# Kernel optimization log

Hardware: AMD Instinct MI355X
Metric: run time of the kernel (lower is better)

Reference implementation:

```python
import jax, jax.numpy as jnp
import numpy as np

N, B, FD, D, MSG, SCN, H, FFN = 2048, 16, 128, 32, 32, 16, 4, 64
HD = D // H


def _lin(k, o, i, scale=0.05):
    kw, kb = jax.random.split(k)
    return (jax.random.normal(kw, (o, i), jnp.float32) * scale,
            jax.random.normal(kb, (o,), jnp.float32) * scale)


def setup_inputs() -> dict:
    key = jax.random.key(0)
    ks = jax.random.split(key, 24)
    inp = {}
    inp['src'] = jax.random.randint(ks[0], (B,), 0, N)
    inp['dst'] = jax.random.randint(ks[1], (B,), 0, N)
    inp['edge_feat'] = jax.random.normal(ks[2], (B, 3), jnp.float32)
    inp['timestamps'] = jax.random.uniform(ks[3], (B,), dtype=jnp.float32)
    inp['node_features'] = jax.random.normal(ks[4], (N, FD), jnp.float32)
    inp['adj'] = jnp.zeros((N, N), jnp.float32)  # unused: assume_identity_adj=True
    inp['memory'] = jax.random.normal(ks[5], (N, D), jnp.float32) * 0.1
    inp['W_emb'], inp['b_emb'] = _lin(ks[6], D, FD)
    inp['Wqkv'], inp['bqkv'] = _lin(ks[7], 3 * D, D)
    inp['Wo'], inp['bo'] = _lin(ks[8], D, D)
    inp['g1'] = jnp.ones((D,), jnp.float32); inp['be1'] = jnp.zeros((D,), jnp.float32)
    inp['g2'] = jnp.ones((D,), jnp.float32); inp['be2'] = jnp.zeros((D,), jnp.float32)
    inp['W_f1'], inp['b_f1'] = _lin(ks[9], FFN, D)
    inp['W_f2'], inp['b_f2'] = _lin(ks[10], D, FFN)
    inp['W_scn'], inp['b_scn'] = _lin(ks[11], SCN, D)
    inp['g_scn'] = jnp.ones((SCN,), jnp.float32); inp['be_scn'] = jnp.zeros((SCN,), jnp.float32)
    inp['W_e1'], inp['b_e1'] = _lin(ks[12], 32, 2 * SCN)
    inp['W_e2'], inp['b_e2'] = _lin(ks[13], 16, 32)
    inp['W_e3'], inp['b_e3'] = _lin(ks[14], 1, 16)
    inp['gru_Wih'], inp['gru_bih'] = _lin(ks[15], 3 * D, MSG)
    inp['gru_Whh'], inp['gru_bhh'] = _lin(ks[16], 3 * D, D)
    inp['W_m1'], inp['b_m1'] = _lin(ks[17], MSG, 2 * D + 3)
    inp['W_m2'], inp['b_m2'] = _lin(ks[18], MSG, MSG)
    return inp


def _ln(x, g, b):
    mu = x.mean(-1, keepdims=True)
    var = ((x - mu) ** 2).mean(-1, keepdims=True)
    return (x - mu) * jax.lax.rsqrt(var + 1e-5) * g + b


def _gru(x, h, Wih, Whh, bih, bhh):
    # torch.nn.GRUCell semantics
    gi = x @ Wih.T + bih
    gh = h @ Whh.T + bhh
    ir, iz, i_n = jnp.split(gi, 3, -1)
    hr, hz, h_n = jnp.split(gh, 3, -1)
    r = jax.nn.sigmoid(ir + hr)
    z = jax.nn.sigmoid(iz + hz)
    n = jnp.tanh(i_n + r * h_n)
    return (1.0 - z) * n + z * h


def _update_memory(memory, src, dst, edge_feat,
                   gru_Wih, gru_Whh, gru_bih, gru_bhh, W_m1, b_m1, W_m2, b_m2):
    # messages computed from pre-update memory (as in torch source)
    msg_in = jnp.concatenate([memory[src], memory[dst], edge_feat], axis=1)  # [B, 2D+3]
    messages = jax.nn.relu(msg_in @ W_m1.T + b_m1) @ W_m2.T + b_m2           # [B, MSG]

    def step(mem, inp):
        s, d, m = inp
        hs = _gru(m, mem[s], gru_Wih, gru_Whh, gru_bih, gru_bhh)
        mem = mem.at[s].set(hs)
        hd = _gru(m, mem[d], gru_Wih, gru_Whh, gru_bih, gru_bhh)  # sees updated mem if d==s earlier
        mem = mem.at[d].set(hd)
        return mem, None

    new_mem, _ = jax.lax.scan(step, memory, (src, dst, messages))
    return new_mem


def _edge_logits(node_features, src, dst,
                 W_emb, b_emb, Wqkv, bqkv, Wo, bo, g1, be1, g2, be2,
                 W_f1, b_f1, W_f2, b_f2, W_scn, b_scn, g_scn, be_scn,
                 W_e1, b_e1, W_e2, b_e2, W_e3, b_e3):
    x0 = node_features @ W_emb.T + b_emb                      # [N, D]
    x = jnp.broadcast_to(x0[None], (B, N, D))                 # [B, N, D]
    # --- Graph transformer layer (MHA, eval mode: dropout = identity) ---
    qkv = x @ Wqkv.T + bqkv                                   # [B, N, 3D]
    q, k, v = jnp.split(qkv, 3, -1)
    q = q.reshape(B, N, H, HD)
    k = k.reshape(B, N, H, HD)
    v = v.reshape(B, N, H, HD)
    scores = jnp.einsum('bqhd,bkhd->bhqk', q, k) / np.sqrt(HD)
    attn = jax.nn.softmax(scores, axis=-1)
    ao = jnp.einsum('bhqk,bkhd->bqhd', attn, v).reshape(B, N, D)
    ao = ao @ Wo.T + bo
    x = _ln(x + ao, g1, be1)
    ffn = jax.nn.gelu(x @ W_f1.T + b_f1, approximate=False) @ W_f2.T + b_f2
    x = _ln(x + ffn, g2, be2)
    # --- SCN layer (identity adjacency assumed) ---
    s_out = jax.nn.relu(_ln(x @ W_scn.T + b_scn, g_scn, be_scn))  # [B, N, SCN]
    bi = jnp.arange(B)
    src_emb = s_out[bi, src]
    dst_emb = s_out[bi, dst]
    h = jnp.concatenate([src_emb, dst_emb], axis=-1)
    h = jax.nn.relu(h @ W_e1.T + b_e1)
    h = jax.nn.relu(h @ W_e2.T + b_e2)
    return (h @ W_e3.T + b_e3).squeeze(-1)                    # [B]


def reference(src, dst, edge_feat, timestamps, node_features, adj, memory,
              W_emb, b_emb, Wqkv, bqkv, Wo, bo, g1, be1, g2, be2,
              W_f1, b_f1, W_f2, b_f2, W_scn, b_scn, g_scn, be_scn,
              W_e1, b_e1, W_e2, b_e2, W_e3, b_e3,
              gru_Wih, gru_bih, gru_Whh, gru_bhh, W_m1, b_m1, W_m2, b_m2):
    new_mem = _update_memory(memory, src, dst, edge_feat,
                             gru_Wih, gru_Whh, gru_bih, gru_bhh,
                             W_m1, b_m1, W_m2, b_m2)
    edge_logit = _edge_logits(node_features, src, dst,
                              W_emb, b_emb, Wqkv, bqkv, Wo, bo, g1, be1, g2, be2,
                              W_f1, b_f1, W_f2, b_f2, W_scn, b_scn, g_scn, be_scn,
                              W_e1, b_e1, W_e2, b_e2, W_e3, b_e3)
    return edge_logit, new_mem
```

## Files before the change

### kernel.cpp

```cpp
#include <hip/hip_runtime.h>
#include <math.h>

#define NN   2048
#define BB   16

#define WS_X0   0
#define WS_QT   65536
#define WS_KT   131072
#define WS_VT   196608
#define WS_PART 262144
#define WS_GI   268800
#define WS_FLAG 270336

__device__ __forceinline__ float sigmoidf_(float x) { return 1.0f / (1.0f + __expf(-x)); }
__device__ __forceinline__ float tanhf_(float x) {
    float ex = __expf(2.0f * x);
    return 1.0f - 2.0f / (ex + 1.0f);
}
__device__ __forceinline__ float dot4_(float4 a, float4 b) {
    return a.x*b.x + a.y*b.y + a.z*b.z + a.w*b.w;
}

__global__ __launch_bounds__(256) void kA_embed_qkv_msg(
    const float* __restrict__ nf, const float* __restrict__ Wemb, const float* __restrict__ bemb,
    const float* __restrict__ Wqkv, const float* __restrict__ bqkv,
    const float* __restrict__ mem, const int* __restrict__ src, const int* __restrict__ dst,
    const float* __restrict__ ef,
    const float* __restrict__ Wm1, const float* __restrict__ bm1,
    const float* __restrict__ Wm2, const float* __restrict__ bm2,
    const float* __restrict__ Wih, const float* __restrict__ bih,
    float* __restrict__ ws, float* __restrict__ out)
{
    __shared__ float We_s[32 * 130];
    __shared__ float nf_s[8 * 130];
    __shared__ float x0_s[8 * 33];
    __shared__ float Wq_s[96 * 33];
    __shared__ __align__(16) float Wm1_s[2144];
    __shared__ float Wm2_s[32 * 33];
    __shared__ float Wih_s[96 * 33];
    __shared__ float min_s[67];
    __shared__ float mr_s[32];
    __shared__ float msg_s[32];

    const int t = threadIdx.x, bx = blockIdx.x;
    const bool domsg = (bx < 16);

    float4 rA[4], rB[3], rC;
    #pragma unroll
    for (int k = 0; k < 4; ++k) rA[k] = ((const float4*)Wemb)[t + 256 * k];
    #pragma unroll
    for (int k = 0; k < 3; ++k) rB[k] = ((const float4*)Wqkv)[t + 256 * k];
    rC = ((const float4*)nf)[bx * 256 + t];

    float4 rm1[3], rm2v, rih[3];
    float rminv = 0.f;
    if (domsg) {
        #pragma unroll
        for (int k = 0; k < 3; ++k) {
            int idx = t + 256 * k;
            rm1[k] = (idx < 536) ? ((const float4*)Wm1)[idx] : make_float4(0,0,0,0);
        }
        rm2v = ((const float4*)Wm2)[t];
        #pragma unroll
        for (int k = 0; k < 3; ++k) rih[k] = ((const float4*)Wih)[t + 256 * k];
        if (t < 67) {
            const int e = bx;
            rminv = (t < 32) ? mem[src[e] * 32 + t]
                  : (t < 64) ? mem[dst[e] * 32 + (t - 32)]
                             : ef[e * 3 + (t - 64)];
        }
    }

    if (bx == 255 && t < 128) ((unsigned*)(ws + WS_FLAG))[t] = 0u;
    if (bx >= 16 && bx < 80) {
        int g = (bx - 16) * 256 + t;
        ((float4*)(out + 16))[g] = ((const float4*)mem)[g];
    }

    #pragma unroll
    for (int k = 0; k < 4; ++k) {
        int idx = t + 256 * k;
        int r = idx >> 5, c = (idx & 31) * 4;
        We_s[r * 130 + c] = rA[k].x; We_s[r * 130 + c + 1] = rA[k].y;
        We_s[r * 130 + c + 2] = rA[k].z; We_s[r * 130 + c + 3] = rA[k].w;
    }
    #pragma unroll
    for (int k = 0; k < 3; ++k) {
        int idx = t + 256 * k;
        int r = idx >> 3, c = (idx & 7) * 4;
        Wq_s[r * 33 + c] = rB[k].x; Wq_s[r * 33 + c + 1] = rB[k].y;
        Wq_s[r * 33 + c + 2] = rB[k].z; Wq_s[r * 33 + c + 3] = rB[k].w;
    }
    {
        int r = t >> 5, c = (t & 31) * 4;
        nf_s[r * 130 + c] = rC.x; nf_s[r * 130 + c + 1] = rC.y;
        nf_s[r * 130 + c + 2] = rC.z; nf_s[r * 130 + c + 3] = rC.w;
    }
    if (domsg) {
        #pragma unroll
        for (int k = 0; k < 3; ++k) {
            int idx = t + 256 * k;
            if (idx < 536) ((float4*)Wm1_s)[idx] = rm1[k];
        }
        { int r = t >> 3, c = (t & 7) * 4;
          Wm2_s[r * 33 + c] = rm2v.x; Wm2_s[r * 33 + c + 1] = rm2v.y;
          Wm2_s[r * 33 + c + 2] = rm2v.z; Wm2_s[r * 33 + c + 3] = rm2v.w; }
        #pragma unroll
        for (int k = 0; k < 3; ++k) {
            int idx = t + 256 * k;
            int r = idx >> 3, c = (idx & 7) * 4;
            Wih_s[r * 33 + c] = rih[k].x; Wih_s[r * 33 + c + 1] = rih[k].y;
            Wih_s[r * 33 + c + 2] = rih[k].z; Wih_s[r * 33 + c + 3] = rih[k].w;
        }
        if (t < 67) min_s[t] = rminv;
    }
    __syncthreads();

    const int j = t >> 5, o = t & 31;
    const int n = bx * 8 + j;

    float acc = bemb[o];
    {
        const float2* Wr = (const float2*)&We_s[o * 130];
        const float2* Nr = (const float2*)&nf_s[j * 130];
        float sx = 0.f, sy = 0.f;
        #pragma unroll 16
        for (int i = 0; i < 64; ++i) {
            float2 w = Wr[i], x = Nr[i];
            sx += w.x * x.x; sy += w.y * x.y;
        }
        acc += sx + sy;
    }
    x0_s[j * 33 + o] = acc;
    ws[WS_X0 + n * 32 + o] = acc;
    if (domsg && t < 32) {
        float a1 = bm1[t];
        for (int i = 0; i < 67; ++i) a1 += Wm1_s[t * 67 + i] * min_s[i];
        mr_s[t] = fmaxf(a1, 0.f);
    }
    __syncthreads();

    #pragma unroll
    for (int c = 0; c < 3; ++c) {
        int oo = c * 32 + o;
        float a2 = bqkv[oo];
        #pragma unroll 8
        for (int i = 0; i < 32; ++i) a2 += Wq_s[oo * 33 + i] * x0_s[j * 33 + i];
        int h = o >> 3, d = o & 7;
        float* base = ws + (c == 0 ? WS_QT : (c == 1 ? WS_KT : WS_VT));
        base[h * 16384 + n * 8 + d] = a2;
    }
    if (domsg && t < 32) {
        float a2 = bm2[t];
        #pragma unroll 8
        for (int i = 0; i < 32; ++i) a2 += Wm2_s[t * 33 + i] * mr_s[i];
        msg_s[t] = a2;
    }
    __syncthreads();

    if (domsg && t < 96) {
        float a3 = bih[t];
        #pragma unroll 8
        for (int i = 0; i < 32; ++i) a3 += Wih_s[t * 33 + i] * msg_s[i];
        ws[WS_GI + bx * 96 + t] = a3;
    }
}

__global__ __launch_bounds__(256, 1) void kB_attn_post_scan(
    const int* __restrict__ src, const int* __restrict__ dst,
    const float* __restrict__ mem,
    const float* __restrict__ Wo, const float* __restrict__ bo,
    const float* __restrict__ g1, const float* __restrict__ be1,
    const float* __restrict__ Wf1, const float* __restrict__ bf1,
    const float* __restrict__ Wf2, const float* __restrict__ bf2,
    const float* __restrict__ g2, const float* __restrict__ be2,
    const float* __restrict__ Wscn, const float* __restrict__ bscn,
    const float* __restrict__ gscn, const float* __restrict__ bescn,
    const float* __restrict__ Whh, const float* __restrict__ bhh,
    const float* __restrict__ We1, const float* __restrict__ be1e,
    const float* __restrict__ We2, const float* __restrict__ be2e,
    const float* __restrict__ We3, const float* __restrict__ be3,
    float* __restrict__ ws, float* __restrict__ out)
{
    __shared__ float Wo_s[32 * 33];
    __shared__ float Wf1_s[64 * 33];
    __shared__ float Wf2_s[32 * 65];
    __shared__ float Ws_s[16 * 33];
    __shared__ float arow[32 * 33];
    __shared__ float x1s[32 * 33];
    __shared__ float fs[32 * 65];
    __shared__ float sout_s[32 * 17];
    __shared__ float We1_s[32 * 33];
    __shared__ float We2_s[16 * 33];
    __shared__ float gi_s[16 * 97];
    __shared__ __align__(16) float slots[32 * 36];
    __shared__ int nid_s[32], fid_s[32], last_s[32];

    const int t = threadIdx.x, bx = blockIdx.x;
    unsigned* flags = (unsigned*)(ws + WS_FLAG);

    float4 w1[8], w2[8], w3[8];
    float b1 = 0.f, b2 = 0.f, b3 = 0.f;
    float4 rWo, rF1a, rF1b, rF2a, rF2b, rE1, rWs, rE2, rG0, rG1;
    if (bx == 0) {
        if (t < 64) {
            const int r2 = (t < 32) ? t + 64 : t - 32;
            const int r3 = t + 32;
            #pragma unroll
            for (int c = 0; c < 8; ++c) {
                w1[c] = ((const float4*)Whh)[t * 8 + c];
                w2[c] = ((const float4*)Whh)[r2 * 8 + c];
                w3[c] = ((const float4*)Whh)[r3 * 8 + c];
            }
            b1 = bhh[t]; b2 = bhh[r2]; b3 = bhh[r3];
        }
        rWo  = ((const float4*)Wo)[t];
        rF1a = ((const float4*)Wf1)[t]; rF1b = ((const float4*)Wf1)[t + 256];
        rF2a = ((const float4*)Wf2)[t]; rF2b = ((const float4*)Wf2)[t + 256];
        rE1  = ((const float4*)We1)[t];
        rG0  = ((const float4*)(ws + WS_GI))[t];
        if (t < 128) {
            rWs = ((const float4*)Wscn)[t];
            rE2 = ((const float4*)We2)[t];
            rG1 = ((const float4*)(ws + WS_GI))[t + 256];
        }
        if (t < 32) nid_s[t] = (t & 1) ? dst[t >> 1] : src[t >> 1];
    }

    {
        const int s  = bx >> 2;
        const int ks = bx & 3;
        const int h  = t >> 6;
        const int l  = t & 63;
        const int e = s >> 1;
        const int n = (s & 1) ? dst[e] : src[e];

        const float* qg = ws + WS_QT + h * 16384 + n * 8;
        const float4 qa  = *(const float4*)qg;
        const float4 qb4 = *(const float4*)(qg + 4);
        const float* kbase = ws + WS_KT + h * 16384;
        const float* vbase = ws + WS_VT + h * 16384;

        float4 oa = make_float4(0.f, 0.f, 0.f, 0.f);
        float4 ob = make_float4(0.f, 0.f, 0.f, 0.f);
        float ssum = 0.f;
        const float scale = 0.35355339059327373f;

        #pragma unroll
        for (int i = 0; i < 8; ++i) {
            const int key = ks * 512 + i * 64 + l;
            const float4 ka = *(const float4*)(kbase + key * 8);
            const float4 kb = *(const float4*)(kbase + key * 8 + 4);
            const float sc = (dot4_(qa, ka) + dot4_(qb4, kb)) * scale;
            const float p = __expf(sc);
            ssum += p;
            const float4 va = *(const float4*)(vbase + key * 8);
            const float4 vb = *(const float4*)(vbase + key * 8 + 4);
            oa.x += p * va.x; oa.y += p * va.y; oa.z += p * va.z; oa.w += p * va.w;
            ob.x += p * vb.x; ob.y += p * vb.y; ob.z += p * vb.z; ob.w += p * vb.w;
        }
        #pragma unroll
        for (int m = 1; m <= 32; m <<= 1) {
            ssum += __shfl_xor(ssum, m);
            oa.x += __shfl_xor(oa.x, m); oa.y += __shfl_xor(oa.y, m);
            oa.z += __shfl_xor(oa.z, m); oa.w += __shfl_xor(oa.w, m);
            ob.x += __shfl_xor(ob.x, m); ob.y += __shfl_xor(ob.y, m);
            ob.z += __shfl_xor(ob.z, m); ob.w += __shfl_xor(ob.w, m);
        }
        if (l == 0) {
            float* p = ws + WS_PART + ((s * 4 + h) * 4 + ks) * 12;
            *(float4*)p       = oa;
            *(float4*)(p + 4) = ob;
            p[8] = ssum;
        }
    }
    __threadfence();
    if (t == 0) atomicExch(&flags[bx], 1u);
    if (bx != 0) return;

    if (t < 128) {
        while (atomicAdd(&flags[t], 0u) == 0u) { __builtin_amdgcn_s_sleep(8); }
    }
    __syncthreads();
    __threadfence();

    const int j0 = t >> 5, o = t & 31;

    { int r = t >> 3, c = (t & 7) * 4;
      Wo_s[r * 33 + c] = rWo.x; Wo_s[r * 33 + c + 1] = rWo.y;
      Wo_s[r * 33 + c + 2] = rWo.z; Wo_s[r * 33 + c + 3] = rWo.w;
      We1_s[r * 33 + c] = rE1.x; We1_s[r * 33 + c + 1] = rE1.y;
      We1_s[r * 33 + c + 2] = rE1.z; We1_s[r * 33 + c + 3] = rE1.w;
      Wf1_s[r * 33 + c] = rF1a.x; Wf1_s[r * 33 + c + 1] = rF1a.y;
      Wf1_s[r * 33 + c + 2] = rF1a.z; Wf1_s[r * 33 + c + 3] = rF1a.w;
      int r2 = (t + 256) >> 3, c2 = ((t + 256) & 7) * 4;
      Wf1_s[r2 * 33 + c2] = rF1b.x; Wf1_s[r2 * 33 + c2 + 1] = rF1b.y;
      Wf1_s[r2 * 33 + c2 + 2] = rF1b.z; Wf1_s[r2 * 33 + c2 + 3] = rF1b.w; }
    { int r = t >> 4, c = (t & 15) * 4;
      Wf2_s[r * 65 + c] = rF2a.x; Wf2_s[r * 65 + c + 1] = rF2a.y;
      Wf2_s[r * 65 + c + 2] = rF2a.z; Wf2_s[r * 65 + c + 3] = rF2a.w;
      int r2 = (t + 256) >> 4, c2 = ((t + 256) & 15) * 4;
      Wf2_s[r2 * 65 + c2] = rF2b.x; Wf2_s[r2 * 65 + c2 + 1] = rF2b.y;
      Wf2_s[r2 * 65 + c2 + 2] = rF2b.z; Wf2_s[r2 * 65 + c2 + 3] = rF2b.w; }
    { int f = 4 * t, e = f / 96, off = f - e * 96;
      gi_s[e * 97 + off] = rG0.x; gi_s[e * 97 + off + 1] = rG0.y;
      gi_s[e * 97 + off + 2] = rG0.z; gi_s[e * 97 + off + 3] = rG0.w; }
    if (t < 128) {
        int r = t >> 3, c = (t & 7) * 4;
        Ws_s[r * 33 + c] = rWs.x; Ws_s[r * 33 + c + 1] = rWs.y;
        Ws_s[r * 33 + c + 2] = rWs.z; Ws_s[r * 33 + c + 3] = rWs.w;
        We2_s[r * 33 + c] = rE2.x; We2_s[r * 33 + c + 1] = rE2.y;
        We2_s[r * 33 + c + 2] = rE2.z; We2_s[r * 33 + c + 3] = rE2.w;
        int f = 4 * (t + 256), e2 = f / 96, off = f - e2 * 96;
        gi_s[e2 * 97 + off] = rG1.x; gi_s[e2 * 97 + off + 1] = rG1.y;
        gi_s[e2 * 97 + off + 2] = rG1.z; gi_s[e2 * 97 + off + 3] = rG1.w;
    }

    float x0v[4];
    #pragma unroll
    for (int si = 0; si < 4; ++si) {
        const int jj = si * 8 + j0;
        const int ej = jj >> 1;
        const int n = (jj & 1) ? dst[ej] : src[ej];
        const int h = o >> 3, d = o & 7;
        float num = 0.f, den = 0.f;
        #pragma unroll
        for (int ks = 0; ks < 4; ++ks) {
            const float* p = ws + WS_PART + ((jj * 4 + h) * 4 + ks) * 12;
            num += p[d];
            den += p[8];
        }
        arow[jj * 33 + o] = num / den;
        x0v[si] = ws[WS_X0 + n * 32 + o];
    }
    __syncthreads();

    if (t < 32) {
        int me = nid_s[t], f = t;
        for (int j2 = 0; j2 < t; ++j2) if (nid_s[j2] == me) { f = j2; break; }
        fid_s[t] = f;
        int isl = 1;
        for (int j2 = t + 1; j2 < 32; ++j2) if (nid_s[j2] == me) { isl = 0; break; }
        last_s[t] = isl;
    }
    __syncthreads();

    #pragma unroll
    for (int k = 0; k < 4; ++k) {
        int j2 = j0 + 8 * k;
        if (fid_s[j2] == j2) slots[j2 * 36 + o] = mem[nid_s[j2] * 32 + o];
    }

    #pragma unroll
    for (int si = 0; si < 4; ++si) {
        const int jj = si * 8 + j0;
        float a = bo[o];
        #pragma unroll 8
        for (int i = 0; i < 32; ++i) a += Wo_s[o * 33 + i] * arow[jj * 33 + i];
        float t1 = x0v[si] + a;
        float mu = t1;
        #pragma unroll
        for (int m = 16; m >= 1; m >>= 1) mu += __shfl_xor(mu, m, 32);
        mu *= (1.f / 32.f);
        float dv = t1 - mu;
        float var = dv * dv;
        #pragma unroll
        for (int m = 16; m >= 1; m >>= 1) var += __shfl_xor(var, m, 32);
        var *= (1.f / 32.f);
        x1s[jj * 33 + o] = dv * rsqrtf(var + 1e-5f) * g1[o] + be1[o];
    }
    __syncthreads();

    #pragma unroll
    for (int si = 0; si < 4; ++si) {
        const int jj = si * 8 + j0;
        #pragma unroll
        for (int c = 0; c < 2; ++c) {
            int oo = c * 32 + o;
            float f = bf1[oo];
            #pragma unroll 8
            for (int i = 0; i < 32; ++i) f += Wf1_s[oo * 33 + i] * x1s[jj * 33 + i];
            fs[jj * 65 + oo] = 0.5f * f * (1.f + erff(f * 0.70710678118654752f));
        }
    }
    __syncthreads();

    #pragma unroll
    for (int si = 0; si < 4; ++si) {
        const int jj = si * 8 + j0;
        float f2 = bf2[o];
        #pragma unroll 8
        for (int i = 0; i < 64; ++i) f2 += Wf2_s[o * 65 + i] * fs[jj * 65 + i];
        float t2 = x1s[jj * 33 + o] + f2;
        float mu2 = t2;
        #pragma unroll
        for (int m = 16; m >= 1; m >>= 1) mu2 += __shfl_xor(mu2, m, 32);
        mu2 *= (1.f / 32.f);
        float dv2 = t2 - mu2;
        float var2 = dv2 * dv2;
        #pragma unroll
        for (int m = 16; m >= 1; m >>= 1) var2 += __shfl_xor(var2, m, 32);
        var2 *= (1.f / 32.f);
        x1s[jj * 33 + o] = dv2 * rsqrtf(var2 + 1e-5f) * g2[o] + be2[o];
    }
    __syncthreads();

    if (o < 16) {
        #pragma unroll
        for (int si = 0; si < 4; ++si) {
            const int jj = si * 8 + j0;
            float sc = bscn[o];
            #pragma unroll 8
            for (int i = 0; i < 32; ++i) sc += Ws_s[o * 33 + i] * x1s[jj * 33 + i];
            float m16 = sc;
            #pragma unroll
            for (int m = 8; m >= 1; m >>= 1) m16 += __shfl_xor(m16, m, 16);
            m16 *= (1.f / 16.f);
            float d16 = sc - m16;
            float v16 = d16 * d16;
            #pragma unroll
            for (int m = 8; m >= 1; m >>= 1) v16 += __shfl_xor(v16, m, 16);
            v16 *= (1.f / 16.f);
            float sv = d16 * rsqrtf(v16 + 1e-5f) * gscn[o] + bescn[o];
            sout_s[jj * 17 + o] = fmaxf(sv, 0.f);
        }
    }
    __syncthreads();

    #pragma unroll
    for (int k = 0; k < 2; ++k) {
        int idx = t + 256 * k;
        int e = idx >> 5, i = idx & 31;
        arow[e * 33 + i] = (i < 16) ? sout_s[(2 * e) * 17 + i]
                                    : sout_s[(2 * e + 1) * 17 + (i - 16)];
    }
    __syncthreads();

    #pragma unroll
    for (int k = 0; k < 2; ++k) {
        int e = j0 + 8 * k;
        float acc = be1e[o];
        #pragma unroll 8
        for (int i = 0; i < 32; ++i) acc += We1_s[o * 33 + i] * arow[e * 33 + i];
        fs[e * 33 + o] = fmaxf(acc, 0.f);
    }
    __syncthreads();

    {
        int e = t >> 4, o2 = t & 15;
        float acc = be2e[o2];
        #pragma unroll 8
        for (int i = 0; i < 32; ++i) acc += We2_s[o2 * 33 + i] * fs[e * 33 + i];
        fs[600 + e * 17 + o2] = fmaxf(acc, 0.f);
    }
    __syncthreads();

    if (t < 16) {
        float acc = be3[0];
        #pragma unroll
        for (int i = 0; i < 16; ++i) acc += We3[i] * fs[600 + t * 17 + i];
        out[t] = acc;
    }
    __syncthreads();

    if (t < 64) {
        const bool lowhalf = (t < 32);
        for (int e = 0; e < 16; ++e) {
            const int js = 2 * e, jd = 2 * e + 1;
            const int ss = fid_s[js], sd = fid_s[jd];
            const bool same = (nid_s[js] == nid_s[jd]);
            const int npass = same ? 2 : 1;
            for (int pass = 0; pass < npass; ++pass) {
                const bool do_src = (!same) || (pass == 0);
                const bool do_dst = (!same) || (pass == 1);
                float acc1 = b1, acc2 = b2, acc3 = b3;
                #pragma unroll
                for (int c = 0; c < 8; ++c) {
                    const float4 hs4 = *(const float4*)&slots[ss * 36 + 4 * c];
                    const float4 hd4 = *(const float4*)&slots[sd * 36 + 4 * c];
                    acc1 += dot4_(w1[c], hs4);
                    const float4 hm = lowhalf ? hs4 : hd4;
                    acc2 += dot4_(w2[c], hm);
                    acc3 += dot4_(w3[c], hd4);
                }
                const float shv = __shfl_xor(lowhalf ? acc3 : acc1, 32);
                const float hr = lowhalf ? acc1 : acc2;
                const float hz = shv;
                const float hn = lowhalf ? acc2 : acc3;
                const float ir  = gi_s[e * 97 + o];
                const float iz  = gi_s[e * 97 + 32 + o];
                const float inn = gi_s[e * 97 + 64 + o];
                const float r = sigmoidf_(ir + hr);
                const float z = sigmoidf_(iz + hz);
                const float nn = tanhf_(inn + r * hn);
                const int slot = lowhalf ? ss : sd;
                const float hold = slots[slot * 36 + o];
                const float hnew = (1.f - z) * nn + z * hold;
                const bool wr = lowhalf ? do_src : do_dst;
                if (wr) slots[slot * 36 + o] = hnew;
                __threadfence_block();
            }
        }
    }
    __syncthreads();

    #pragma unroll
    for (int k = 0; k < 4; ++k) {
        int j2 = j0 + 8 * k;
        if (last_s[j2]) out[16 + nid_s[j2] * 32 + o] = slots[fid_s[j2] * 36 + o];
    }
}

extern "C" void kernel_launch(void* const* d_in, const int* in_sizes, int n_in,
                              void* d_out, int out_size, void* d_ws, size_t ws_size,
                              hipStream_t stream)
{
    (void)in_sizes; (void)n_in; (void)out_size; (void)ws_size;
    const int*   src   = (const int*)d_in[0];
    const int*   dst   = (const int*)d_in[1];
    const float* ef    = (const float*)d_in[2];
    const float* nf    = (const float*)d_in[4];
    const float* mem   = (const float*)d_in[6];
    const float* Wemb  = (const float*)d_in[7];
    const float* bemb  = (const float*)d_in[8];
    const float* Wqkv  = (const float*)d_in[9];
    const float* bqkv  = (const float*)d_in[10];
    const float* Wo    = (const float*)d_in[11];
    const float* bo    = (const float*)d_in[12];
    const float* g1    = (const float*)d_in[13];
    const float* be1   = (const float*)d_in[14];
    const float* g2    = (const float*)d_in[15];
    const float* be2   = (const float*)d_in[16];
    const float* Wf1   = (const float*)d_in[17];
    const float* bf1   = (const float*)d_in[18];
    const float* Wf2   = (const float*)d_in[19];
    const float* bf2   = (const float*)d_in[20];
    const float* Wscn  = (const float*)d_in[21];
    const float* bscn  = (const float*)d_in[22];
    const float* gscn  = (const float*)d_in[23];
    const float* bescn = (const float*)d_in[24];
    const float* We1   = (const float*)d_in[25];
    const float* be1e  = (const float*)d_in[26];
    const float* We2   = (const float*)d_in[27];
    const float* be2e  = (const float*)d_in[28];
    const float* We3   = (const float*)d_in[29];
    const float* be3   = (const float*)d_in[30];
    const float* Wih   = (const float*)d_in[31];
    const float* bih   = (const float*)d_in[32];
    const float* Whh   = (const float*)d_in[33];
    const float* bhh   = (const float*)d_in[34];
    const float* Wm1   = (const float*)d_in[35];
    const float* bm1   = (const float*)d_in[36];
    const float* Wm2   = (const float*)d_in[37];
    const float* bm2   = (const float*)d_in[38];
    float* out = (float*)d_out;
    float* ws  = (float*)d_ws;

    hipLaunchKernelGGL(kA_embed_qkv_msg, dim3(256), dim3(256), 0, stream,
        nf, Wemb, bemb, Wqkv, bqkv, mem, src, dst, ef, Wm1, bm1, Wm2, bm2, Wih, bih, ws, out);
    hipLaunchKernelGGL(kB_attn_post_scan, dim3(128), dim3(256), 0, stream,
        src, dst, mem, Wo, bo, g1, be1, Wf1, bf1, Wf2, bf2, g2, be2,
        Wscn, bscn, gscn, bescn, Whh, bhh, We1, be1e, We2, be2e, We3, be3, ws, out);
}
```

Measured before the change: 184.6 us.

## Split attention into its own kernel and parallelize GRU scan by dependency rounds

The fused attention+tail kernel, which used a global flag spin-wait so block 0 could run the serial tail, is split into a separate 128-block attention kernel and a single-block post/scan kernel. This removes the cross-block atomic polling at the cost of an extra launch. The GRU memory update no longer walks 16 edges serially. It now computes dependency rounds per node occurrence and processes all independent slot updates of a round in parallel across the four wavefronts. Small bias vectors are staged in shared memory, and the scan-output shuffle stage is folded into a direct write.

```diff
diff --git a/kernel.cpp b/kernel.cpp
--- a/kernel.cpp
+++ b/kernel.cpp
@@ -10,7 +10,21 @@
 #define WS_VT   196608
 #define WS_PART 262144
 #define WS_GI   268800
-#define WS_FLAG 270336
+
+#define B_BO    0
+#define B_G1    32
+#define B_BE1   64
+#define B_G2    96
+#define B_BE2   128
+#define B_BF1   160
+#define B_BF2   224
+#define B_BSCN  256
+#define B_GSCN  272
+#define B_BESCN 288
+#define B_BE1E  304
+#define B_BE2E  336
+#define B_WE3   352
+#define B_BE3   368
 
 __device__ __forceinline__ float sigmoidf_(float x) { return 1.0f / (1.0f + __expf(-x)); }
 __device__ __forceinline__ float tanhf_(float x) {
@@ -21,7 +35,7 @@
     return a.x*b.x + a.y*b.y + a.z*b.z + a.w*b.w;
 }
 
-__global__ __launch_bounds__(256) void kA_embed_qkv_msg(
+__global__ __launch_bounds__(256) void k1_embed_qkv_msg(
     const float* __restrict__ nf, const float* __restrict__ Wemb, const float* __restrict__ bemb,
     const float* __restrict__ Wqkv, const float* __restrict__ bqkv,
     const float* __restrict__ mem, const int* __restrict__ src, const int* __restrict__ dst,
@@ -71,7 +85,6 @@
         }
     }
 
-    if (bx == 255 && t < 128) ((unsigned*)(ws + WS_FLAG))[t] = 0u;
     if (bx >= 16 && bx < 80) {
         int g = (bx - 16) * 256 + t;
         ((float4*)(out + 16))[g] = ((const float4*)mem)[g];
@@ -166,7 +179,61 @@
     }
 }
 
-__global__ __launch_bounds__(256, 1) void kB_attn_post_scan(
+__global__ __launch_bounds__(256) void k2_attn(
+    const int* __restrict__ src, const int* __restrict__ dst,
+    float* __restrict__ ws)
+{
+    const int t = threadIdx.x, bx = blockIdx.x;
+    const int s  = bx >> 2;
+    const int ks = bx & 3;
+    const int h  = t >> 6;
+    const int l  = t & 63;
+
+    const int e = s >> 1;
+    const int n = (s & 1) ? dst[e] : src[e];
+
+    const float* qg = ws + WS_QT + h * 16384 + n * 8;
+    const float4 qa  = *(const float4*)qg;
+    const float4 qb4 = *(const float4*)(qg + 4);
+    const float* kbase = ws + WS_KT + h * 16384;
+    const float* vbase = ws + WS_VT + h * 16384;
+
+    float4 oa = make_float4(0.f, 0.f, 0.f, 0.f);
+    float4 ob = make_float4(0.f, 0.f, 0.f, 0.f);
+    float ssum = 0.f;
+    const float scale = 0.35355339059327373f;
+
+    #pragma unroll
+    for (int i = 0; i < 8; ++i) {
+        const int key = ks * 512 + i * 64 + l;
+        const float4 ka = *(const float4*)(kbase + key * 8);
+        const float4 kb = *(const float4*)(kbase + key * 8 + 4);
+        const float sc = (dot4_(qa, ka) + dot4_(qb4, kb)) * scale;
+        const float p = __expf(sc);
+        ssum += p;
+        const float4 va = *(const float4*)(vbase + key * 8);
+        const float4 vb = *(const float4*)(vbase + key * 8 + 4);
+        oa.x += p * va.x; oa.y += p * va.y; oa.z += p * va.z; oa.w += p * va.w;
+        ob.x += p * vb.x; ob.y += p * vb.y; ob.z += p * vb.z; ob.w += p * vb.w;
+    }
+
+    #pragma unroll
+    for (int m = 1; m <= 32; m <<= 1) {
+        ssum += __shfl_xor(ssum, m);
+        oa.x += __shfl_xor(oa.x, m); oa.y += __shfl_xor(oa.y, m);
+        oa.z += __shfl_xor(oa.z, m); oa.w += __shfl_xor(oa.w, m);
+        ob.x += __shfl_xor(ob.x, m); ob.y += __shfl_xor(ob.y, m);
+        ob.z += __shfl_xor(ob.z, m); ob.w += __shfl_xor(ob.w, m);
+    }
+    if (l == 0) {
+        float* p = ws + WS_PART + ((s * 4 + h) * 4 + ks) * 12;
+        *(float4*)p       = oa;
+        *(float4*)(p + 4) = ob;
+        p[8] = ssum;
+    }
+}
+
+__global__ __launch_bounds__(256, 1) void k34_post_scan(
     const int* __restrict__ src, const int* __restrict__ dst,
     const float* __restrict__ mem,
     const float* __restrict__ Wo, const float* __restrict__ bo,
@@ -186,105 +253,66 @@
     __shared__ float Wf1_s[64 * 33];
     __shared__ float Wf2_s[32 * 65];
     __shared__ float Ws_s[16 * 33];
+    __shared__ float We1_s[32 * 33];
+    __shared__ float We2_s[16 * 33];
     __shared__ float arow[32 * 33];
     __shared__ float x1s[32 * 33];
     __shared__ float fs[32 * 65];
-    __shared__ float sout_s[32 * 17];
-    __shared__ float We1_s[32 * 33];
-    __shared__ float We2_s[16 * 33];
     __shared__ float gi_s[16 * 97];
     __shared__ __align__(16) float slots[32 * 36];
-    __shared__ int nid_s[32], fid_s[32], last_s[32];
-
-    const int t = threadIdx.x, bx = blockIdx.x;
-    unsigned* flags = (unsigned*)(ws + WS_FLAG);
+    __shared__ float bias_s[384];
+    __shared__ int nid_s[32], prev_s[32], round_s[32], last_s[32];
+    __shared__ int list_s[32], cnt_s, maxr_s;
+
+    const int t = threadIdx.x;
+    const int j0 = t >> 5, o = t & 31;
+    const int l = t & 63, w = t >> 6;
+    const bool lowhalf = (l < 32);
 
     float4 w1[8], w2[8], w3[8];
-    float b1 = 0.f, b2 = 0.f, b3 = 0.f;
+    {
+        const int r2 = lowhalf ? l + 64 : l - 32;
+        const int r3 = l + 32;
+        #pragma unroll
+        for (int c = 0; c < 8; ++c) {
+            w1[c] = ((const float4*)Whh)[l * 8 + c];
+            w2[c] = ((const float4*)Whh)[r2 * 8 + c];
+            w3[c] = ((const float4*)Whh)[r3 * 8 + c];
+        }
+    }
+    const float b1 = bhh[l], b2 = bhh[lowhalf ? l + 64 : l - 32], b3 = bhh[l + 32];
+
     float4 rWo, rF1a, rF1b, rF2a, rF2b, rE1, rWs, rE2, rG0, rG1;
-    if (bx == 0) {
-        if (t < 64) {
-            const int r2 = (t < 32) ? t + 64 : t - 32;
-            const int r3 = t + 32;
-            #pragma unroll
-            for (int c = 0; c < 8; ++c) {
-                w1[c] = ((const float4*)Whh)[t * 8 + c];
-                w2[c] = ((const float4*)Whh)[r2 * 8 + c];
-                w3[c] = ((const float4*)Whh)[r3 * 8 + c];
-            }
-            b1 = bhh[t]; b2 = bhh[r2]; b3 = bhh[r3];
-        }
-        rWo  = ((const float4*)Wo)[t];
-        rF1a = ((const float4*)Wf1)[t]; rF1b = ((const float4*)Wf1)[t + 256];
-        rF2a = ((const float4*)Wf2)[t]; rF2b = ((const float4*)Wf2)[t + 256];
-        rE1  = ((const float4*)We1)[t];
-        rG0  = ((const float4*)(ws + WS_GI))[t];
-        if (t < 128) {
-            rWs = ((const float4*)Wscn)[t];
-            rE2 = ((const float4*)We2)[t];
-            rG1 = ((const float4*)(ws + WS_GI))[t + 256];
-        }
-        if (t < 32) nid_s[t] = (t & 1) ? dst[t >> 1] : src[t >> 1];
-    }
-
-    {
-        const int s  = bx >> 2;
-        const int ks = bx & 3;
-        const int h  = t >> 6;
-        const int l  = t & 63;
-        const int e = s >> 1;
-        const int n = (s & 1) ? dst[e] : src[e];
-
-        const float* qg = ws + WS_QT + h * 16384 + n * 8;
-        const float4 qa  = *(const float4*)qg;
-        const float4 qb4 = *(const float4*)(qg + 4);
-        const float* kbase = ws + WS_KT + h * 16384;
-        const float* vbase = ws + WS_VT + h * 16384;
-
-        float4 oa = make_float4(0.f, 0.f, 0.f, 0.f);
-        float4 ob = make_float4(0.f, 0.f, 0.f, 0.f);
-        float ssum = 0.f;
-        const float scale = 0.35355339059327373f;
-
-        #pragma unroll
-        for (int i = 0; i < 8; ++i) {
-            const int key = ks * 512 + i * 64 + l;
-            const float4 ka = *(const float4*)(kbase + key * 8);
-            const float4 kb = *(const float4*)(kbase + key * 8 + 4);
-            const float sc = (dot4_(qa, ka) + dot4_(qb4, kb)) * scale;
-            const float p = __expf(sc);
-            ssum += p;
-            const float4 va = *(const float4*)(vbase + key * 8);
-            const float4 vb = *(const float4*)(vbase + key * 8 + 4);
-            oa.x += p * va.x; oa.y += p * va.y; oa.z += p * va.z; oa.w += p * va.w;
-            ob.x += p * vb.x; ob.y += p * vb.y; ob.z += p * vb.z; ob.w += p * vb.w;
-        }
-        #pragma unroll
-        for (int m = 1; m <= 32; m <<= 1) {
-            ssum += __shfl_xor(ssum, m);
-            oa.x += __shfl_xor(oa.x, m); oa.y += __shfl_xor(oa.y, m);
-            oa.z += __shfl_xor(oa.z, m); oa.w += __shfl_xor(oa.w, m);
-            ob.x += __shfl_xor(ob.x, m); ob.y += __shfl_xor(ob.y, m);
-            ob.z += __shfl_xor(ob.z, m); ob.w += __shfl_xor(ob.w, m);
-        }
-        if (l == 0) {
-            float* p = ws + WS_PART + ((s * 4 + h) * 4 + ks) * 12;
-            *(float4*)p       = oa;
-            *(float4*)(p + 4) = ob;
-            p[8] = ssum;
-        }
-    }
-    __threadfence();
-    if (t == 0) atomicExch(&flags[bx], 1u);
-    if (bx != 0) return;
-
+    rWo  = ((const float4*)Wo)[t];
+    rF1a = ((const float4*)Wf1)[t]; rF1b = ((const float4*)Wf1)[t + 256];
+    rF2a = ((const float4*)Wf2)[t]; rF2b = ((const float4*)Wf2)[t + 256];
+    rE1  = ((const float4*)We1)[t];
+    rG0  = ((const float4*)(ws + WS_GI))[t];
     if (t < 128) {
-        while (atomicAdd(&flags[t], 0u) == 0u) { __builtin_amdgcn_s_sleep(8); }
-    }
-    __syncthreads();
-    __threadfence();
-
-    const int j0 = t >> 5, o = t & 31;
+        rWs = ((const float4*)Wscn)[t];
+        rE2 = ((const float4*)We2)[t];
+        rG1 = ((const float4*)(ws + WS_GI))[t + 256];
+    }
+    if (t < 32) {
+        bias_s[B_BO + t]   = bo[t];
+        bias_s[B_G1 + t]   = g1[t];
+        bias_s[B_BE1 + t]  = be1[t];
+        bias_s[B_G2 + t]   = g2[t];
+        bias_s[B_BE2 + t]  = be2[t];
+        bias_s[B_BF1 + t]  = bf1[t];
+        bias_s[B_BF1 + 32 + t] = bf1[32 + t];
+        bias_s[B_BF2 + t]  = bf2[t];
+        bias_s[B_BE1E + t] = be1e[t];
+        nid_s[t] = (t & 1) ? dst[t >> 1] : src[t >> 1];
+    }
+    if (t < 16) {
+        bias_s[B_BSCN + t]  = bscn[t];
+        bias_s[B_GSCN + t]  = gscn[t];
+        bias_s[B_BESCN + t] = bescn[t];
+        bias_s[B_BE2E + t]  = be2e[t];
+        bias_s[B_WE3 + t]   = We3[t];
+    }
+    if (t == 0) bias_s[B_BE3] = be3[0];
 
     { int r = t >> 3, c = (t & 7) * 4;
       Wo_s[r * 33 + c] = rWo.x; Wo_s[r * 33 + c + 1] = rWo.y;
@@ -336,25 +364,28 @@
     __syncthreads();
 
     if (t < 32) {
-        int me = nid_s[t], f = t;
-        for (int j2 = 0; j2 < t; ++j2) if (nid_s[j2] == me) { f = j2; break; }
-        fid_s[t] = f;
+        const int me = nid_s[t];
+        int pv = -1, rd = 0;
+        for (int j2 = 0; j2 < t; ++j2) if (nid_s[j2] == me) { pv = j2; ++rd; }
+        prev_s[t] = pv; round_s[t] = rd;
         int isl = 1;
         for (int j2 = t + 1; j2 < 32; ++j2) if (nid_s[j2] == me) { isl = 0; break; }
         last_s[t] = isl;
-    }
-    __syncthreads();
-
+        int mr = rd;
+        #pragma unroll
+        for (int m = 16; m >= 1; m >>= 1) mr = max(mr, __shfl_xor(mr, m, 32));
+        if (t == 0) maxr_s = mr;
+    }
     #pragma unroll
     for (int k = 0; k < 4; ++k) {
         int j2 = j0 + 8 * k;
-        if (fid_s[j2] == j2) slots[j2 * 36 + o] = mem[nid_s[j2] * 32 + o];
+        slots[j2 * 36 + o] = mem[nid_s[j2] * 32 + o];
     }
 
     #pragma unroll
     for (int si = 0; si < 4; ++si) {
         const int jj = si * 8 + j0;
-        float a = bo[o];
+        float a = bias_s[B_BO + o];
         #pragma unroll 8
         for (int i = 0; i < 32; ++i) a += Wo_s[o * 33 + i] * arow[jj * 33 + i];
         float t1 = x0v[si] + a;
@@ -367,7 +398,7 @@
         #pragma unroll
         for (int m = 16; m >= 1; m >>= 1) var += __shfl_xor(var, m, 32);
         var *= (1.f / 32.f);
-        x1s[jj * 33 + o] = dv * rsqrtf(var + 1e-5f) * g1[o] + be1[o];
+        x1s[jj * 33 + o] = dv * rsqrtf(var + 1e-5f) * bias_s[B_G1 + o] + bias_s[B_BE1 + o];
     }
     __syncthreads();
 
@@ -377,7 +408,7 @@
         #pragma unroll
         for (int c = 0; c < 2; ++c) {
             int oo = c * 32 + o;
-            float f = bf1[oo];
+            float f = bias_s[B_BF1 + oo];
             #pragma unroll 8
             for (int i = 0; i < 32; ++i) f += Wf1_s[oo * 33 + i] * x1s[jj * 33 + i];
             fs[jj * 65 + oo] = 0.5f * f * (1.f + erff(f * 0.70710678118654752f));
@@ -388,7 +419,7 @@
     #pragma unroll
     for (int si = 0; si < 4; ++si) {
         const int jj = si * 8 + j0;
-        float f2 = bf2[o];
+        float f2 = bias_s[B_BF2 + o];
         #pragma unroll 8
         for (int i = 0; i < 64; ++i) f2 += Wf2_s[o * 65 + i] * fs[jj * 65 + i];
         float t2 = x1s[jj * 33 + o] + f2;
@@ -401,7 +432,7 @@
         #pragma unroll
         for (int m = 16; m >= 1; m >>= 1) var2 += __shfl_xor(var2, m, 32);
         var2 *= (1.f / 32.f);
-        x1s[jj * 33 + o] = dv2 * rsqrtf(var2 + 1e-5f) * g2[o] + be2[o];
+        x1s[jj * 33 + o] = dv2 * rsqrtf(var2 + 1e-5f) * bias_s[B_G2 + o] + bias_s[B_BE2 + o];
     }
     __syncthreads();
 
@@ -409,7 +440,7 @@
         #pragma unroll
         for (int si = 0; si < 4; ++si) {
             const int jj = si * 8 + j0;
-            float sc = bscn[o];
+            float sc = bias_s[B_BSCN + o];
             #pragma unroll 8
             for (int i = 0; i < 32; ++i) sc += Ws_s[o * 33 + i] * x1s[jj * 33 + i];
             float m16 = sc;
@@ -421,25 +452,16 @@
             #pragma unroll
             for (int m = 8; m >= 1; m >>= 1) v16 += __shfl_xor(v16, m, 16);
             v16 *= (1.f / 16.f);
-            float sv = d16 * rsqrtf(v16 + 1e-5f) * gscn[o] + bescn[o];
-            sout_s[jj * 17 + o] = fmaxf(sv, 0.f);
-        }
-    }
-    __syncthreads();
-
-    #pragma unroll
-    for (int k = 0; k < 2; ++k) {
-        int idx = t + 256 * k;
-        int e = idx >> 5, i = idx & 31;
-        arow[e * 33 + i] = (i < 16) ? sout_s[(2 * e) * 17 + i]
-                                    : sout_s[(2 * e + 1) * 17 + (i - 16)];
+            float sv = d16 * rsqrtf(v16 + 1e-5f) * bias_s[B_GSCN + o] + bias_s[B_BESCN + o];
+            arow[(jj >> 1) * 33 + (jj & 1) * 16 + o] = fmaxf(sv, 0.f);
+        }
     }
     __syncthreads();
 
     #pragma unroll
     for (int k = 0; k < 2; ++k) {
         int e = j0 + 8 * k;
-        float acc = be1e[o];
+        float acc = bias_s[B_BE1E + o];
         #pragma unroll 8
         for (int i = 0; i < 32; ++i) acc += We1_s[o * 33 + i] * arow[e * 33 + i];
         fs[e * 33 + o] = fmaxf(acc, 0.f);
@@ -448,7 +470,7 @@
 
     {
         int e = t >> 4, o2 = t & 15;
-        float acc = be2e[o2];
+        float acc = bias_s[B_BE2E + o2];
         #pragma unroll 8
         for (int i = 0; i < 32; ++i) acc += We2_s[o2 * 33 + i] * fs[e * 33 + i];
         fs[600 + e * 17 + o2] = fmaxf(acc, 0.f);
@@ -456,58 +478,64 @@
     __syncthreads();
 
     if (t < 16) {
-        float acc = be3[0];
-        #pragma unroll
-        for (int i = 0; i < 16; ++i) acc += We3[i] * fs[600 + t * 17 + i];
+        float acc = bias_s[B_BE3];
+        #pragma unroll
+        for (int i = 0; i < 16; ++i) acc += bias_s[B_WE3 + i] * fs[600 + t * 17 + i];
         out[t] = acc;
     }
-    __syncthreads();
-
-    if (t < 64) {
-        const bool lowhalf = (t < 32);
-        for (int e = 0; e < 16; ++e) {
-            const int js = 2 * e, jd = 2 * e + 1;
-            const int ss = fid_s[js], sd = fid_s[jd];
-            const bool same = (nid_s[js] == nid_s[jd]);
-            const int npass = same ? 2 : 1;
-            for (int pass = 0; pass < npass; ++pass) {
-                const bool do_src = (!same) || (pass == 0);
-                const bool do_dst = (!same) || (pass == 1);
-                float acc1 = b1, acc2 = b2, acc3 = b3;
-                #pragma unroll
-                for (int c = 0; c < 8; ++c) {
-                    const float4 hs4 = *(const float4*)&slots[ss * 36 + 4 * c];
-                    const float4 hd4 = *(const float4*)&slots[sd * 36 + 4 * c];
-                    acc1 += dot4_(w1[c], hs4);
-                    const float4 hm = lowhalf ? hs4 : hd4;
-                    acc2 += dot4_(w2[c], hm);
-                    acc3 += dot4_(w3[c], hd4);
-                }
-                const float shv = __shfl_xor(lowhalf ? acc3 : acc1, 32);
-                const float hr = lowhalf ? acc1 : acc2;
-                const float hz = shv;
-                const float hn = lowhalf ? acc2 : acc3;
-                const float ir  = gi_s[e * 97 + o];
-                const float iz  = gi_s[e * 97 + 32 + o];
-                const float inn = gi_s[e * 97 + 64 + o];
-                const float r = sigmoidf_(ir + hr);
-                const float z = sigmoidf_(iz + hz);
-                const float nn = tanhf_(inn + r * hn);
-                const int slot = lowhalf ? ss : sd;
-                const float hold = slots[slot * 36 + o];
-                const float hnew = (1.f - z) * nn + z * hold;
-                const bool wr = lowhalf ? do_src : do_dst;
-                if (wr) slots[slot * 36 + o] = hnew;
-                __threadfence_block();
+
+    const int maxr = maxr_s;
+    for (int r = 0; r <= maxr; ++r) {
+        if (t < 64) {
+            bool act = (t < 32) && (round_s[t] == r);
+            unsigned long long mask = __ballot(act);
+            if (act) {
+                int pos = __popcll(mask & ((1ull << t) - 1ull));
+                list_s[pos] = t;
             }
-        }
-    }
-    __syncthreads();
+            if (t == 0) cnt_s = (int)__popcll(mask);
+        }
+        __syncthreads();
+        const int cnt = cnt_s;
+        for (int pi = w; 2 * pi < cnt; pi += 4) {
+            const int sA = list_s[2 * pi];
+            const bool doB = (2 * pi + 1 < cnt);
+            const int sB = doB ? list_s[2 * pi + 1] : sA;
+            const int inA = (prev_s[sA] < 0) ? sA : prev_s[sA];
+            const int inB = (prev_s[sB] < 0) ? sB : prev_s[sB];
+            float acc1 = b1, acc2 = b2, acc3 = b3;
+            #pragma unroll
+            for (int c = 0; c < 8; ++c) {
+                const float4 hs4 = *(const float4*)&slots[inA * 36 + 4 * c];
+                const float4 hd4 = *(const float4*)&slots[inB * 36 + 4 * c];
+                acc1 += dot4_(w1[c], hs4);
+                const float4 hm = lowhalf ? hs4 : hd4;
+                acc2 += dot4_(w2[c], hm);
+                acc3 += dot4_(w3[c], hd4);
+            }
+            const float shv = __shfl_xor(lowhalf ? acc3 : acc1, 32);
+            const float hr = lowhalf ? acc1 : acc2;
+            const float hz = shv;
+            const float hn = lowhalf ? acc2 : acc3;
+            const int sX = lowhalf ? sA : sB;
+            const int eX = sX >> 1;
+            const float ir  = gi_s[eX * 97 + o];
+            const float iz  = gi_s[eX * 97 + 32 + o];
+            const float inn = gi_s[eX * 97 + 64 + o];
+            const float rr = sigmoidf_(ir + hr);
+            const float z = sigmoidf_(iz + hz);
+            const float nn = tanhf_(inn + rr * hn);
+            const float hold = slots[(lowhalf ? inA : inB) * 36 + o];
+            const float hnew = (1.f - z) * nn + z * hold;
+            if (lowhalf || doB) slots[sX * 36 + o] = hnew;
+        }
+        __syncthreads();
+    }
 
     #pragma unroll
     for (int k = 0; k < 4; ++k) {
         int j2 = j0 + 8 * k;
-        if (last_s[j2]) out[16 + nid_s[j2] * 32 + o] = slots[fid_s[j2] * 36 + o];
+        if (last_s[j2]) out[16 + nid_s[j2] * 32 + o] = slots[j2 * 36 + o];
     }
 }
 
@@ -556,9 +584,10 @@
     float* out = (float*)d_out;
     float* ws  = (float*)d_ws;
 
-    hipLaunchKernelGGL(kA_embed_qkv_msg, dim3(256), dim3(256), 0, stream,
+    hipLaunchKernelGGL(k1_embed_qkv_msg, dim3(256), dim3(256), 0, stream,
         nf, Wemb, bemb, Wqkv, bqkv, mem, src, dst, ef, Wm1, bm1, Wm2, bm2, Wih, bih, ws, out);
-    hipLaunchKernelGGL(kB_attn_post_scan, dim3(128), dim3(256), 0, stream,
+    hipLaunchKernelGGL(k2_attn, dim3(128), dim3(256), 0, stream, src, dst, ws);
+    hipLaunchKernelGGL(k34_post_scan, dim3(1), dim3(256), 0, stream,
         src, dst, mem, Wo, bo, g1, be1, Wf1, bf1, Wf2, bf2, g2, be2,
         Wscn, bscn, gscn, bescn, Whh, bhh, We1, be1e, We2, be2e, We3, be3, ws, out);
 }
```

Measured after the change: 174.2 us. 5.6% less time.
